# Kernel optimization log

Hardware: AMD Instinct MI355X
Metric: run time of the kernel (lower is better)

Reference implementation:

```python
import jax, jax.numpy as jnp
import numpy as np

N_GRAPHS = 128   # number of graphs in the batch
G = 128          # nodes per graph (equal-sized ragged blocks for the reference)
D = 512          # node embedding dim (feature_dim)
EPS = 1e-7


def setup_inputs() -> dict:
    key = jax.random.key(0)
    embeddings = jax.random.normal(key, (N_GRAPHS * G, D), dtype=jnp.float32)
    # Precompute block-diagonal strict-upper-triangular mask as gather indices.
    # Equivalent to torch.block_diag(*[triu(ones(g,g), diagonal=1) for g in sizes]).bool()
    iu_r, iu_c = np.triu_indices(G, k=1)                 # per-block triu(.,1) indices
    offsets = (np.arange(N_GRAPHS) * G)[:, None]         # block offsets into [N, N]
    row_idx = jnp.asarray((offsets + iu_r[None, :]).ravel(), dtype=jnp.int32)
    col_idx = jnp.asarray((offsets + iu_c[None, :]).ravel(), dtype=jnp.int32)
    return {"embeddings": embeddings, "row_idx": row_idx, "col_idx": col_idx}


def reference(embeddings, row_idx, col_idx):
    # Full NxN dot-product similarity (N = total nodes across all graphs).
    sims = embeddings @ embeddings.T                     # [N, N]
    m = sims.min()
    M = sims.max()
    sims = (sims - m) / (M - m + EPS)                    # global min-max normalization
    # Gather block-diagonal strict-upper-triangular entries -> flat vector.
    return sims[row_idx, col_idx]                        # [sum_g g*(g-1)/2]
```

## Files before the change

### kernel.cpp

```cpp
#include <hip/hip_runtime.h>
#include <hip/hip_bf16.h>
#include <stdint.h>


typedef __attribute__((ext_vector_type(8))) __bf16 bf16x8;
typedef __attribute__((ext_vector_type(16))) float floatx16;
typedef __attribute__((ext_vector_type(4))) int intx4;
typedef __attribute__((ext_vector_type(16))) int intx16;

#define AS1 __attribute__((address_space(1)))
#define AS3 __attribute__((address_space(3)))

static constexpr int DIM      = 512;
static constexpr int NTILE    = 128;
static constexpr int GX       = 72;
static constexpr int NPAIRIDX = 65 * 128;
static constexpr float QS     = 19.5f;
static constexpr int MARGIN_I = 3042;


static __device__ __forceinline__ unsigned short f2bf_rne(float f) {
  unsigned int u = __float_as_uint(f);
  u += 0x7fffu + ((u >> 16) & 1u);
  return (unsigned short)(u >> 16);
}
static __device__ __forceinline__ int fkey(float f) {
  int s = __float_as_int(f);
  return s >= 0 ? s : (s ^ 0x7fffffff);
}
static __device__ __forceinline__ float funkey(int k) {
  return __int_as_float(k >= 0 ? k : (k ^ 0x7fffffff));
}
static __device__ __forceinline__ int swzd(int row, int c16) {
  return c16 ^ (row & 15);
}
static __device__ __forceinline__ int swz8(int row, int c8) {
  return c8 ^ (row & 7);
}
static __device__ __forceinline__ int qswap(int v) {
  return (v & 0x7A) | ((v & 1) << 2) | ((v >> 2) & 1);
}
static __device__ __forceinline__ int sfun(int row) {
  return (row & 3) ^ ((row >> 3) & 3);
}

__global__ void k_convert(const float* __restrict__ in,
                          unsigned short* __restrict__ bf,
                          char* __restrict__ q,
                          int* __restrict__ ctrl, int n4) {
  int i = blockIdx.x * blockDim.x + threadIdx.x;
  if (i == 0) {
    ctrl[0] = 0x7fffffff; ctrl[1] = (int)0x80000000;
    ctrl[2] = 0x7fffffff;
  }
  if (i >= n4) return;
  float4 v = ((const float4*)in)[i];
  ushort4 o;
  o.x = f2bf_rne(v.x); o.y = f2bf_rne(v.y);
  o.z = f2bf_rne(v.z); o.w = f2bf_rne(v.w);
  ((ushort4*)bf)[i] = o;
  int qx = __float2int_rn(v.x * QS), qy = __float2int_rn(v.y * QS);
  int qz = __float2int_rn(v.z * QS), qw = __float2int_rn(v.w * QS);
  char4 c;
  c.x = (char)min(127, max(-127, qx));
  c.y = (char)min(127, max(-127, qy));
  c.z = (char)min(127, max(-127, qz));
  c.w = (char)min(127, max(-127, qw));
  ((char4*)q)[i] = c;
}

__global__ __launch_bounds__(256, 4) void k_gemm(
    const char* __restrict__ Eq,
    const unsigned short* __restrict__ E,
    int* __restrict__ ipart,
    float* __restrict__ diagblocks,
    int* __restrict__ ctrl) {
  const int x  = blockIdx.x;
  const int tr = blockIdx.y;
  if (x > 64) return;
  const int pi = tr * 65 + x;

  const int tid = threadIdx.x;
  __shared__ __align__(16) char smem[2][16384];
  __shared__ float2 redbuf[4];
  __shared__ int iredbuf[4];

  const int w = tid >> 6, lane = tid & 63;
  const int wr = w >> 1, wc = w & 1;
  const int l31 = lane & 31;
  const int kg  = lane >> 5;

  if (x < 64) {
    const int tcw = (tr + 1 + x) & 127;
    const int a = min(tr, tcw), b = max(tr, tcw);
    const int rowA = a * 128;
    const int rowB = b * 128;

    intx16 acc[2][2];
#pragma unroll
    for (int i = 0; i < 2; i++)
#pragma unroll
      for (int j = 0; j < 2; j++)
#pragma unroll
        for (int r = 0; r < 16; r++) acc[i][j][r] = 0;

#define STAGE4(bb, kt) do {                                                   \
    _Pragma("unroll")                                                         \
    for (int jj_ = 0; jj_ < 2; jj_++) {                                       \
      int p_   = jj_ * 256 + tid;                                             \
      int q_   = p_ >> 2;                                                     \
      int row_ = qswap(q_);                                                   \
      int off_ = (kt) * 64 + (((p_ & 3) ^ sfun(row_)) * 16);                  \
      char* d_ = smem[bb] + p_ * 16;                                          \
      __builtin_amdgcn_global_load_lds(                                       \
          (const AS1 unsigned int*)(Eq + (size_t)(rowA + row_) * DIM + off_), \
          (AS3 unsigned int*)d_, 16, 0, 0);                                   \
      __builtin_amdgcn_global_load_lds(                                       \
          (const AS1 unsigned int*)(Eq + (size_t)(rowB + row_) * DIM + off_), \
          (AS3 unsigned int*)(d_ + 8192), 16, 0, 0);                          \
    }                                                                         \
  } while (0)

    const int ra0 = wr * 64 + l31,  ra1 = wr * 64 + 32 + l31;
    const int rb0 = wc * 64 + l31,  rb1 = wc * 64 + 32 + l31;
    const int pa0 = qswap(ra0) * 64, sa0 = sfun(ra0);
    const int pa1 = qswap(ra1) * 64, sa1 = sfun(ra1);
    const int pb0 = qswap(rb0) * 64, sb0 = sfun(rb0);
    const int pb1 = qswap(rb1) * 64, sb1 = sfun(rb1);

    STAGE4(0, 0);
    __syncthreads();

#pragma unroll
    for (int kt = 0; kt < 8; kt++) {
      if (kt + 1 < 8) STAGE4((kt + 1) & 1, kt + 1);
      const char* cb = smem[kt & 1];
#pragma unroll
      for (int ks = 0; ks < 2; ks++) {
        const int c = ks * 2 + kg;
        intx4 af0 = *(const intx4*)(cb +        pa0 + ((c ^ sa0) << 4));
        intx4 af1 = *(const intx4*)(cb +        pa1 + ((c ^ sa1) << 4));
        intx4 bf0 = *(const intx4*)(cb + 8192 + pb0 + ((c ^ sb0) << 4));
        intx4 bf1 = *(const intx4*)(cb + 8192 + pb1 + ((c ^ sb1) << 4));
        acc[0][0] = __builtin_amdgcn_mfma_i32_32x32x32_i8(af0, bf0, acc[0][0], 0, 0, 0);
        acc[0][1] = __builtin_amdgcn_mfma_i32_32x32x32_i8(af0, bf1, acc[0][1], 0, 0, 0);
        acc[1][0] = __builtin_amdgcn_mfma_i32_32x32x32_i8(af1, bf0, acc[1][0], 0, 0, 0);
        acc[1][1] = __builtin_amdgcn_mfma_i32_32x32x32_i8(af1, bf1, acc[1][1], 0, 0, 0);
      }
      __syncthreads();
    }
#undef STAGE4

    int vmin = 0x7fffffff;
#pragma unroll
    for (int ti = 0; ti < 2; ti++)
#pragma unroll
      for (int tj = 0; tj < 2; tj++)
#pragma unroll
        for (int r = 0; r < 16; r++) vmin = min(vmin, acc[ti][tj][r]);
#pragma unroll
    for (int m_ = 32; m_ >= 1; m_ >>= 1)
      vmin = min(vmin, __shfl_xor(vmin, m_));
    if (lane == 0) iredbuf[w] = vmin;
    __syncthreads();
    if (tid == 0) {
      int mn = iredbuf[0];
      for (int i = 1; i < 4; i++) mn = min(mn, iredbuf[i]);
      ipart[pi] = mn;
      atomicMin(&ctrl[2], mn);
    }
  } else {
    if (tid == 0) ipart[pi] = 0x7fffffff;
    unsigned short* lA = (unsigned short*)&smem[0][0];
    floatx16 acc[2][2];
#pragma unroll
    for (int i = 0; i < 2; i++)
#pragma unroll
      for (int j = 0; j < 2; j++)
#pragma unroll
        for (int r = 0; r < 16; r++) acc[i][j][r] = 0.f;

    const int rowBase = tr * 128;

    for (int kb = 0; kb < 4; kb++) {
      const int kBase = kb * 128;
#pragma unroll
      for (int j = 0; j < 8; j++) {
        int p   = (w * 8 + j) * 64 + lane;
        int row = p >> 4, c16 = p & 15;
        int sc = swzd(row, c16);
        const unsigned short* gA =
            E + (size_t)(rowBase + row) * DIM + kBase + sc * 8;
        __builtin_amdgcn_global_load_lds((const AS1 unsigned int*)gA,
                                         (AS3 unsigned int*)(lA + p * 8), 16, 0, 0);
      }
      __syncthreads();

#pragma unroll
      for (int ks = 0; ks < 8; ks++) {
        bf16x8 af[2], bfv[2];
        const int c16 = ks * 2 + kg;
#pragma unroll
        for (int t = 0; t < 2; t++) {
          int ra = wr * 64 + t * 32 + l31;
          int rb = wc * 64 + t * 32 + l31;
          af[t]  = *(const bf16x8*)(lA + ra * 128 + swzd(ra, c16) * 8);
          bfv[t] = *(const bf16x8*)(lA + rb * 128 + swzd(rb, c16) * 8);
        }
#pragma unroll
        for (int ti = 0; ti < 2; ti++)
#pragma unroll
          for (int tj = 0; tj < 2; tj++)
            acc[ti][tj] = __builtin_amdgcn_mfma_f32_32x32x16_bf16(
                af[ti], bfv[tj], acc[ti][tj], 0, 0, 0);
      }
      __syncthreads();
    }

    float vmin = 3.4e38f, vmax = -3.4e38f;
#pragma unroll
    for (int ti = 0; ti < 2; ti++)
#pragma unroll
      for (int tj = 0; tj < 2; tj++)
#pragma unroll
        for (int r = 0; r < 16; r++) {
          float v = acc[ti][tj][r];
          vmin = fminf(vmin, v);
          vmax = fmaxf(vmax, v);
        }
#pragma unroll
    for (int m_ = 32; m_ >= 1; m_ >>= 1) {
      vmin = fminf(vmin, __shfl_xor(vmin, m_));
      vmax = fmaxf(vmax, __shfl_xor(vmax, m_));
    }
    if (lane == 0) redbuf[w] = make_float2(vmin, vmax);
    __syncthreads();
    if (tid == 0) {
      float mn = redbuf[0].x, mx = redbuf[0].y;
      for (int i = 1; i < 4; i++) {
        mn = fminf(mn, redbuf[i].x);
        mx = fmaxf(mx, redbuf[i].y);
      }
      atomicMin(&ctrl[0], fkey(mn));
      atomicMax(&ctrl[1], fkey(mx));
    }

    float* Bout = diagblocks + (size_t)tr * (128 * 128);
#pragma unroll
    for (int ti = 0; ti < 2; ti++) {
#pragma unroll
      for (int tj = 0; tj < 2; tj++) {
        int cbase = wc * 64 + tj * 32 + l31;
#pragma unroll
        for (int r = 0; r < 16; r++) {
          int row = wr * 64 + ti * 32 + (r & 3) + 8 * (r >> 2) + 4 * kg;
          Bout[row * 128 + cbase] = acc[ti][tj][r];
        }
      }
    }
  }
}

__global__ __launch_bounds__(256) void k_refine(
    const unsigned short* __restrict__ E,
    const int* __restrict__ ipart, int* __restrict__ ctrl) {
  const int pi = blockIdx.x;
  if (ipart[pi] > ctrl[2] + MARGIN_I) return;
  const int tr = pi / 65, x = pi % 65;
  if (x == 64) return;
  const int tcw = (tr + 1 + x) & 127;
  const int a = min(tr, tcw), b = max(tr, tcw);

  const int tid = threadIdx.x;
  __shared__ __align__(16) unsigned short lA[128 * 64];
  __shared__ __align__(16) unsigned short lB[128 * 64];
  __shared__ float redbuf[4];

  const int w = tid >> 6, lane = tid & 63;
  const int wr = w >> 1, wc = w & 1;
  const int l31 = lane & 31;
  const int kg  = lane >> 5;

  floatx16 acc[2][2];
#pragma unroll
  for (int i = 0; i < 2; i++)
#pragma unroll
    for (int j = 0; j < 2; j++)
#pragma unroll
      for (int r = 0; r < 16; r++) acc[i][j][r] = 0.f;

  const int rowBaseA = a * 128;
  const int rowBaseB = b * 128;

  for (int kb = 0; kb < 8; kb++) {
    const int kBase = kb * 64;
#pragma unroll
    for (int j = 0; j < 4; j++) {
      int cb  = (w * 4 + j) * 64;
      int p   = cb + lane;
      int row = p >> 3, c8 = p & 7;
      int sc8 = swz8(row, c8);
      const unsigned short* gA = E + (size_t)(rowBaseA + row) * DIM + kBase + sc8 * 8;
      const unsigned short* gB = E + (size_t)(rowBaseB + row) * DIM + kBase + sc8 * 8;
      __builtin_amdgcn_global_load_lds((const AS1 unsigned int*)gA,
                                       (AS3 unsigned int*)(lA + cb * 8), 16, 0, 0);
      __builtin_amdgcn_global_load_lds((const AS1 unsigned int*)gB,
                                       (AS3 unsigned int*)(lB + cb * 8), 16, 0, 0);
    }
    __syncthreads();

#pragma unroll
    for (int ks = 0; ks < 4; ks++) {
      bf16x8 af[2], bfv[2];
      const int c8 = ks * 2 + kg;
#pragma unroll
      for (int t = 0; t < 2; t++) {
        int ra = wr * 64 + t * 32 + l31;
        int rb = wc * 64 + t * 32 + l31;
        af[t]  = *(const bf16x8*)(lA + (ra * 8 + swz8(ra, c8)) * 8);
        bfv[t] = *(const bf16x8*)(lB + (rb * 8 + swz8(rb, c8)) * 8);
      }
#pragma unroll
      for (int ti = 0; ti < 2; ti++)
#pragma unroll
        for (int tj = 0; tj < 2; tj++)
          acc[ti][tj] = __builtin_amdgcn_mfma_f32_32x32x16_bf16(
              af[ti], bfv[tj], acc[ti][tj], 0, 0, 0);
    }
    __syncthreads();
  }

  float vmin = 3.4e38f;
#pragma unroll
  for (int ti = 0; ti < 2; ti++)
#pragma unroll
    for (int tj = 0; tj < 2; tj++)
#pragma unroll
      for (int r = 0; r < 16; r++) vmin = fminf(vmin, acc[ti][tj][r]);
#pragma unroll
  for (int m_ = 32; m_ >= 1; m_ >>= 1)
    vmin = fminf(vmin, __shfl_xor(vmin, m_));
  if (lane == 0) redbuf[w] = vmin;
  __syncthreads();
  if (tid == 0) {
    float mn = redbuf[0];
    for (int i = 1; i < 4; i++) mn = fminf(mn, redbuf[i]);
    atomicMin(&ctrl[0], fkey(mn));
  }
}

__global__ __launch_bounds__(256) void k_gather(
    const int* __restrict__ rix, const int* __restrict__ cix,
    const float* __restrict__ blocks, const int* __restrict__ ctrl,
    float* __restrict__ out, int n) {
  int i = blockIdx.x * blockDim.x + threadIdx.x;
  if (i >= n) return;
  float m   = funkey(ctrl[0]);
  float M   = funkey(ctrl[1]);
  float inv = 1.0f / (M - m + 1e-7f);
  int r = rix[i], c = cix[i];
  int g = r >> 7;
  float v = blocks[((size_t)g << 14) + ((r & 127) << 7) + (c & 127)];
  out[i] = (v - m) * inv;
}

extern "C" void kernel_launch(void* const* d_in, const int* in_sizes, int n_in,
                              void* d_out, int out_size, void* d_ws, size_t ws_size,
                              hipStream_t stream) {
  const float* emb = (const float*)d_in[0];
  const int* rix   = (const int*)d_in[1];
  const int* cix   = (const int*)d_in[2];

  char* ws = (char*)d_ws;
  int* ctrl           = (int*)ws;
  unsigned short* Ebf = (unsigned short*)(ws + 256);
  char* Eq            = (char*)(ws + 256 + (16u << 20));
  float* diagblocks   = (float*)(ws + 256 + (24u << 20));
  int* ipart          = (int*)(ws + 256 + (32u << 20));

  int n4 = in_sizes[0] / 4;

  k_convert<<<(n4 + 255) / 256, 256, 0, stream>>>(emb, Ebf, Eq, ctrl, n4);

  k_gemm<<<dim3(GX, 128), 256, 0, stream>>>(Eq, Ebf, ipart, diagblocks, ctrl);

  k_refine<<<NPAIRIDX, 256, 0, stream>>>(Ebf, ipart, ctrl);

  k_gather<<<(out_size + 255) / 256, 256, 0, stream>>>(rix, cix, diagblocks,
                                                       ctrl, (float*)d_out,
                                                       out_size);
}
```

Measured before the change: 219.6 us.

## Compute two column tiles per block in the int8 triangle GEMM with 512 threads

Replaces the circulant one-pair-per-block mapping with an upper-triangular mapping. Each 512-thread block loads one row tile once and computes it against two adjacent column tiles, so the A-tile load and LDS staging are shared across two products. Blocks whose column tiles fall in the lower triangle exit early. The refine kernel and the diagonal bf16 path are remapped to match, with the diagonal path split across 8 waves. This trades A-operand reuse and fewer tile loads for larger LDS use per block, uneven work across the grid, and possible occupancy loss at 512 threads.

Measured after the change: 191.4 us, median of 2. -12.9%, faster.

```diff
diff --git a/kernel.cpp b/kernel.cpp
--- a/kernel.cpp
+++ b/kernel.cpp
@@ -69,7 +69,7 @@
   ((char4*)q)[i] = c;
 }
 
-__global__ __launch_bounds__(256, 4) void k_gemm(
+__global__ __launch_bounds__(512, 4) void k_gemm(
     const char* __restrict__ Eq,
     const unsigned short* __restrict__ E,
     int* __restrict__ ipart,
@@ -81,20 +81,29 @@
   const int pi = tr * 65 + x;
 
   const int tid = threadIdx.x;
-  __shared__ __align__(16) char smem[2][16384];
-  __shared__ float2 redbuf[4];
-  __shared__ int iredbuf[4];
+  __shared__ __align__(16) char smem[2][24576];
+  __shared__ float2 redbuf[8];
+  __shared__ int iredbuf[8];
 
   const int w = tid >> 6, lane = tid & 63;
-  const int wr = w >> 1, wc = w & 1;
   const int l31 = lane & 31;
   const int kg  = lane >> 5;
 
   if (x < 64) {
-    const int tcw = (tr + 1 + x) & 127;
-    const int a = min(tr, tcw), b = max(tr, tcw);
-    const int rowA = a * 128;
-    const int rowB = b * 128;
+    const int tc1 = 2 * x + 1;
+    if (tc1 <= tr) {
+      if (tid == 0) ipart[pi] = 0x7fffffff;
+      return;
+    }
+    const int tc0 = (2 * x > tr) ? 2 * x : tc1;
+
+    const int rowA  = tr  * 128;
+    const int rowB0 = tc0 * 128;
+    const int rowB1 = tc1 * 128;
+
+    const int wr = w >> 2;
+    const int wcq = w & 3;
+    const int bplane = 8192 + (wcq >> 1) * 8192;
 
     intx16 acc[2][2];
 #pragma unroll
@@ -104,44 +113,44 @@
 #pragma unroll
         for (int r = 0; r < 16; r++) acc[i][j][r] = 0;
 
-#define STAGE4(bb, kt) do {                                                   \
-    _Pragma("unroll")                                                         \
-    for (int jj_ = 0; jj_ < 2; jj_++) {                                       \
-      int p_   = jj_ * 256 + tid;                                             \
-      int q_   = p_ >> 2;                                                     \
-      int row_ = qswap(q_);                                                   \
-      int off_ = (kt) * 64 + (((p_ & 3) ^ sfun(row_)) * 16);                  \
-      char* d_ = smem[bb] + p_ * 16;                                          \
-      __builtin_amdgcn_global_load_lds(                                       \
-          (const AS1 unsigned int*)(Eq + (size_t)(rowA + row_) * DIM + off_), \
-          (AS3 unsigned int*)d_, 16, 0, 0);                                   \
-      __builtin_amdgcn_global_load_lds(                                       \
-          (const AS1 unsigned int*)(Eq + (size_t)(rowB + row_) * DIM + off_), \
-          (AS3 unsigned int*)(d_ + 8192), 16, 0, 0);                          \
-    }                                                                         \
+#define STAGE3(bb, kt) do {                                                   \
+    int p_   = tid;                                                           \
+    int q_   = p_ >> 2;                                                       \
+    int row_ = qswap(q_);                                                     \
+    int off_ = (kt) * 64 + (((p_ & 3) ^ sfun(row_)) * 16);                    \
+    char* d_ = smem[bb] + p_ * 16;                                            \
+    __builtin_amdgcn_global_load_lds(                                         \
+        (const AS1 unsigned int*)(Eq + (size_t)(rowA + row_) * DIM + off_),   \
+        (AS3 unsigned int*)d_, 16, 0, 0);                                     \
+    __builtin_amdgcn_global_load_lds(                                         \
+        (const AS1 unsigned int*)(Eq + (size_t)(rowB0 + row_) * DIM + off_),  \
+        (AS3 unsigned int*)(d_ + 8192), 16, 0, 0);                            \
+    __builtin_amdgcn_global_load_lds(                                         \
+        (const AS1 unsigned int*)(Eq + (size_t)(rowB1 + row_) * DIM + off_),  \
+        (AS3 unsigned int*)(d_ + 16384), 16, 0, 0);                           \
   } while (0)
 
-    const int ra0 = wr * 64 + l31,  ra1 = wr * 64 + 32 + l31;
-    const int rb0 = wc * 64 + l31,  rb1 = wc * 64 + 32 + l31;
+    const int ra0 = wr * 64 + l31,        ra1 = wr * 64 + 32 + l31;
+    const int rb0 = (wcq & 1) * 64 + l31, rb1 = (wcq & 1) * 64 + 32 + l31;
     const int pa0 = qswap(ra0) * 64, sa0 = sfun(ra0);
     const int pa1 = qswap(ra1) * 64, sa1 = sfun(ra1);
     const int pb0 = qswap(rb0) * 64, sb0 = sfun(rb0);
     const int pb1 = qswap(rb1) * 64, sb1 = sfun(rb1);
 
-    STAGE4(0, 0);
+    STAGE3(0, 0);
     __syncthreads();
 
 #pragma unroll
     for (int kt = 0; kt < 8; kt++) {
-      if (kt + 1 < 8) STAGE4((kt + 1) & 1, kt + 1);
+      if (kt + 1 < 8) STAGE3((kt + 1) & 1, kt + 1);
       const char* cb = smem[kt & 1];
 #pragma unroll
       for (int ks = 0; ks < 2; ks++) {
         const int c = ks * 2 + kg;
-        intx4 af0 = *(const intx4*)(cb +        pa0 + ((c ^ sa0) << 4));
-        intx4 af1 = *(const intx4*)(cb +        pa1 + ((c ^ sa1) << 4));
-        intx4 bf0 = *(const intx4*)(cb + 8192 + pb0 + ((c ^ sb0) << 4));
-        intx4 bf1 = *(const intx4*)(cb + 8192 + pb1 + ((c ^ sb1) << 4));
+        intx4 af0 = *(const intx4*)(cb +           pa0 + ((c ^ sa0) << 4));
+        intx4 af1 = *(const intx4*)(cb +           pa1 + ((c ^ sa1) << 4));
+        intx4 bf0 = *(const intx4*)(cb + bplane +  pb0 + ((c ^ sb0) << 4));
+        intx4 bf1 = *(const intx4*)(cb + bplane +  pb1 + ((c ^ sb1) << 4));
         acc[0][0] = __builtin_amdgcn_mfma_i32_32x32x32_i8(af0, bf0, acc[0][0], 0, 0, 0);
         acc[0][1] = __builtin_amdgcn_mfma_i32_32x32x32_i8(af0, bf1, acc[0][1], 0, 0, 0);
         acc[1][0] = __builtin_amdgcn_mfma_i32_32x32x32_i8(af1, bf0, acc[1][0], 0, 0, 0);
@@ -149,7 +158,7 @@
       }
       __syncthreads();
     }
-#undef STAGE4
+#undef STAGE3
 
     int vmin = 0x7fffffff;
 #pragma unroll
@@ -165,28 +174,27 @@
     __syncthreads();
     if (tid == 0) {
       int mn = iredbuf[0];
-      for (int i = 1; i < 4; i++) mn = min(mn, iredbuf[i]);
+      for (int i = 1; i < 8; i++) mn = min(mn, iredbuf[i]);
       ipart[pi] = mn;
       atomicMin(&ctrl[2], mn);
     }
   } else {
     if (tid == 0) ipart[pi] = 0x7fffffff;
     unsigned short* lA = (unsigned short*)&smem[0][0];
-    floatx16 acc[2][2];
-#pragma unroll
-    for (int i = 0; i < 2; i++)
-#pragma unroll
-      for (int j = 0; j < 2; j++)
-#pragma unroll
-        for (int r = 0; r < 16; r++) acc[i][j][r] = 0.f;
+    const int wr = w >> 2, wcq = w & 3;
+    floatx16 acc[2];
+#pragma unroll
+    for (int t = 0; t < 2; t++)
+#pragma unroll
+      for (int r = 0; r < 16; r++) acc[t][r] = 0.f;
 
     const int rowBase = tr * 128;
 
     for (int kb = 0; kb < 4; kb++) {
       const int kBase = kb * 128;
 #pragma unroll
-      for (int j = 0; j < 8; j++) {
-        int p   = (w * 8 + j) * 64 + lane;
+      for (int j = 0; j < 4; j++) {
+        int p   = j * 512 + tid;
         int row = p >> 4, c16 = p & 15;
         int sc = swzd(row, c16);
         const unsigned short* gA =
@@ -198,36 +206,34 @@
 
 #pragma unroll
       for (int ks = 0; ks < 8; ks++) {
-        bf16x8 af[2], bfv[2];
+        bf16x8 af[2], bfv;
         const int c16 = ks * 2 + kg;
 #pragma unroll
         for (int t = 0; t < 2; t++) {
           int ra = wr * 64 + t * 32 + l31;
-          int rb = wc * 64 + t * 32 + l31;
           af[t]  = *(const bf16x8*)(lA + ra * 128 + swzd(ra, c16) * 8);
-          bfv[t] = *(const bf16x8*)(lA + rb * 128 + swzd(rb, c16) * 8);
         }
-#pragma unroll
-        for (int ti = 0; ti < 2; ti++)
-#pragma unroll
-          for (int tj = 0; tj < 2; tj++)
-            acc[ti][tj] = __builtin_amdgcn_mfma_f32_32x32x16_bf16(
-                af[ti], bfv[tj], acc[ti][tj], 0, 0, 0);
+        {
+          int rb = wcq * 32 + l31;
+          bfv = *(const bf16x8*)(lA + rb * 128 + swzd(rb, c16) * 8);
+        }
+#pragma unroll
+        for (int t = 0; t < 2; t++)
+          acc[t] = __builtin_amdgcn_mfma_f32_32x32x16_bf16(
+              af[t], bfv, acc[t], 0, 0, 0);
       }
       __syncthreads();
     }
 
     float vmin = 3.4e38f, vmax = -3.4e38f;
 #pragma unroll
-    for (int ti = 0; ti < 2; ti++)
-#pragma unroll
-      for (int tj = 0; tj < 2; tj++)
-#pragma unroll
-        for (int r = 0; r < 16; r++) {
-          float v = acc[ti][tj][r];
-          vmin = fminf(vmin, v);
-          vmax = fmaxf(vmax, v);
-        }
+    for (int t = 0; t < 2; t++)
+#pragma unroll
+      for (int r = 0; r < 16; r++) {
+        float v = acc[t][r];
+        vmin = fminf(vmin, v);
+        vmax = fmaxf(vmax, v);
+      }
 #pragma unroll
     for (int m_ = 32; m_ >= 1; m_ >>= 1) {
       vmin = fminf(vmin, __shfl_xor(vmin, m_));
@@ -237,7 +243,7 @@
     __syncthreads();
     if (tid == 0) {
       float mn = redbuf[0].x, mx = redbuf[0].y;
-      for (int i = 1; i < 4; i++) {
+      for (int i = 1; i < 8; i++) {
         mn = fminf(mn, redbuf[i].x);
         mx = fmaxf(mx, redbuf[i].y);
       }
@@ -246,16 +252,13 @@
     }
 
     float* Bout = diagblocks + (size_t)tr * (128 * 128);
-#pragma unroll
-    for (int ti = 0; ti < 2; ti++) {
-#pragma unroll
-      for (int tj = 0; tj < 2; tj++) {
-        int cbase = wc * 64 + tj * 32 + l31;
-#pragma unroll
-        for (int r = 0; r < 16; r++) {
-          int row = wr * 64 + ti * 32 + (r & 3) + 8 * (r >> 2) + 4 * kg;
-          Bout[row * 128 + cbase] = acc[ti][tj][r];
-        }
+    const int cbase = wcq * 32 + l31;
+#pragma unroll
+    for (int t = 0; t < 2; t++) {
+#pragma unroll
+      for (int r = 0; r < 16; r++) {
+        int row = wr * 64 + t * 32 + (r & 3) + 8 * (r >> 2) + 4 * kg;
+        Bout[row * 128 + cbase] = acc[t][r];
       }
     }
   }
@@ -268,8 +271,6 @@
   if (ipart[pi] > ctrl[2] + MARGIN_I) return;
   const int tr = pi / 65, x = pi % 65;
   if (x == 64) return;
-  const int tcw = (tr + 1 + x) & 127;
-  const int a = min(tr, tcw), b = max(tr, tcw);
 
   const int tid = threadIdx.x;
   __shared__ __align__(16) unsigned short lA[128 * 64];
@@ -281,71 +282,77 @@
   const int l31 = lane & 31;
   const int kg  = lane >> 5;
 
-  floatx16 acc[2][2];
-#pragma unroll
-  for (int i = 0; i < 2; i++)
-#pragma unroll
-    for (int j = 0; j < 2; j++)
-#pragma unroll
-      for (int r = 0; r < 16; r++) acc[i][j][r] = 0.f;
-
-  const int rowBaseA = a * 128;
-  const int rowBaseB = b * 128;
-
-  for (int kb = 0; kb < 8; kb++) {
-    const int kBase = kb * 64;
-#pragma unroll
-    for (int j = 0; j < 4; j++) {
-      int cb  = (w * 4 + j) * 64;
-      int p   = cb + lane;
-      int row = p >> 3, c8 = p & 7;
-      int sc8 = swz8(row, c8);
-      const unsigned short* gA = E + (size_t)(rowBaseA + row) * DIM + kBase + sc8 * 8;
-      const unsigned short* gB = E + (size_t)(rowBaseB + row) * DIM + kBase + sc8 * 8;
-      __builtin_amdgcn_global_load_lds((const AS1 unsigned int*)gA,
-                                       (AS3 unsigned int*)(lA + cb * 8), 16, 0, 0);
-      __builtin_amdgcn_global_load_lds((const AS1 unsigned int*)gB,
-                                       (AS3 unsigned int*)(lB + cb * 8), 16, 0, 0);
-    }
-    __syncthreads();
-
-#pragma unroll
-    for (int ks = 0; ks < 4; ks++) {
-      bf16x8 af[2], bfv[2];
-      const int c8 = ks * 2 + kg;
-#pragma unroll
-      for (int t = 0; t < 2; t++) {
-        int ra = wr * 64 + t * 32 + l31;
-        int rb = wc * 64 + t * 32 + l31;
-        af[t]  = *(const bf16x8*)(lA + (ra * 8 + swz8(ra, c8)) * 8);
-        bfv[t] = *(const bf16x8*)(lB + (rb * 8 + swz8(rb, c8)) * 8);
-      }
-#pragma unroll
-      for (int ti = 0; ti < 2; ti++)
-#pragma unroll
-        for (int tj = 0; tj < 2; tj++)
-          acc[ti][tj] = __builtin_amdgcn_mfma_f32_32x32x16_bf16(
-              af[ti], bfv[tj], acc[ti][tj], 0, 0, 0);
-    }
-    __syncthreads();
-  }
-
-  float vmin = 3.4e38f;
-#pragma unroll
-  for (int ti = 0; ti < 2; ti++)
-#pragma unroll
-    for (int tj = 0; tj < 2; tj++)
-#pragma unroll
-      for (int r = 0; r < 16; r++) vmin = fminf(vmin, acc[ti][tj][r]);
-#pragma unroll
-  for (int m_ = 32; m_ >= 1; m_ >>= 1)
-    vmin = fminf(vmin, __shfl_xor(vmin, m_));
-  if (lane == 0) redbuf[w] = vmin;
-  __syncthreads();
-  if (tid == 0) {
-    float mn = redbuf[0];
-    for (int i = 1; i < 4; i++) mn = fminf(mn, redbuf[i]);
-    atomicMin(&ctrl[0], fkey(mn));
+  for (int s = 0; s < 2; s++) {
+    const int tc = 2 * x + s;
+    if (tc <= tr) continue;
+
+    floatx16 acc[2][2];
+#pragma unroll
+    for (int i = 0; i < 2; i++)
+#pragma unroll
+      for (int j = 0; j < 2; j++)
+#pragma unroll
+        for (int r = 0; r < 16; r++) acc[i][j][r] = 0.f;
+
+    const int rowBaseA = tr * 128;
+    const int rowBaseB = tc * 128;
+
+    for (int kb = 0; kb < 8; kb++) {
+      const int kBase = kb * 64;
+#pragma unroll
+      for (int j = 0; j < 4; j++) {
+        int cb  = (w * 4 + j) * 64;
+        int p   = cb + lane;
+        int row = p >> 3, c8 = p & 7;
+        int sc8 = swz8(row, c8);
+        const unsigned short* gA = E + (size_t)(rowBaseA + row) * DIM + kBase + sc8 * 8;
+        const unsigned short* gB = E + (size_t)(rowBaseB + row) * DIM + kBase + sc8 * 8;
+        __builtin_amdgcn_global_load_lds((const AS1 unsigned int*)gA,
+                                         (AS3 unsigned int*)(lA + cb * 8), 16, 0, 0);
+        __builtin_amdgcn_global_load_lds((const AS1 unsigned int*)gB,
+                                         (AS3 unsigned int*)(lB + cb * 8), 16, 0, 0);
+      }
+      __syncthreads();
+
+#pragma unroll
+      for (int ks = 0; ks < 4; ks++) {
+        bf16x8 af[2], bfv[2];
+        const int c8 = ks * 2 + kg;
+#pragma unroll
+        for (int t = 0; t < 2; t++) {
+          int ra = wr * 64 + t * 32 + l31;
+          int rb = wc * 64 + t * 32 + l31;
+          af[t]  = *(const bf16x8*)(lA + (ra * 8 + swz8(ra, c8)) * 8);
+          bfv[t] = *(const bf16x8*)(lB + (rb * 8 + swz8(rb, c8)) * 8);
+        }
+#pragma unroll
+        for (int ti = 0; ti < 2; ti++)
+#pragma unroll
+          for (int tj = 0; tj < 2; tj++)
+            acc[ti][tj] = __builtin_amdgcn_mfma_f32_32x32x16_bf16(
+                af[ti], bfv[tj], acc[ti][tj], 0, 0, 0);
+      }
+      __syncthreads();
+    }
+
+    float vmin = 3.4e38f;
+#pragma unroll
+    for (int ti = 0; ti < 2; ti++)
+#pragma unroll
+      for (int tj = 0; tj < 2; tj++)
+#pragma unroll
+        for (int r = 0; r < 16; r++) vmin = fminf(vmin, acc[ti][tj][r]);
+#pragma unroll
+    for (int m_ = 32; m_ >= 1; m_ >>= 1)
+      vmin = fminf(vmin, __shfl_xor(vmin, m_));
+    if (lane == 0) redbuf[w] = vmin;
+    __syncthreads();
+    if (tid == 0) {
+      float mn = redbuf[0];
+      for (int i = 1; i < 4; i++) mn = fminf(mn, redbuf[i]);
+      atomicMin(&ctrl[0], fkey(mn));
+    }
+    __syncthreads();
   }
 }
 
@@ -382,7 +389,7 @@
 
   k_convert<<<(n4 + 255) / 256, 256, 0, stream>>>(emb, Ebf, Eq, ctrl, n4);
 
-  k_gemm<<<dim3(GX, 128), 256, 0, stream>>>(Eq, Ebf, ipart, diagblocks, ctrl);
+  k_gemm<<<dim3(GX, 128), 512, 0, stream>>>(Eq, Ebf, ipart, diagblocks, ctrl);
 
   k_refine<<<NPAIRIDX, 256, 0, stream>>>(Ebf, ipart, ctrl);
 
```
